# Performance work log

Measured on AMD Instinct MI355X. Metric: run time of the kernel, lower is better.

The kernel has to match this reference:

```python
import jax, jax.numpy as jnp
import numpy as np

N = 500000
D = 128
R = D // 4  # reduction = 4
G = 2048    # number of graphs


def setup_inputs() -> dict:
    key = jax.random.key(0)
    ks = jax.random.split(key, 8)
    x = jax.random.normal(ks[0], (N, D), dtype=jnp.float32)
    batch = jnp.sort(jax.random.randint(ks[1], (N,), 0, G))
    # SE-gate MLP params (nn.Linear stores weight as [out,in]; we store transposed for x @ W)
    fc_w1 = jax.random.normal(ks[2], (D, R), dtype=jnp.float32) * (1.0 / np.sqrt(D))
    fc_b1 = jnp.zeros((R,), dtype=jnp.float32)
    fc_w2 = jax.random.normal(ks[3], (R, D), dtype=jnp.float32) * (1.0 / np.sqrt(R))
    fc_b2 = jnp.zeros((D,), dtype=jnp.float32)
    # xavier-uniform weight_matrix [D, D]
    lim = np.sqrt(6.0 / (D + D))
    W = jax.random.uniform(ks[4], (D, D), dtype=jnp.float32, minval=-lim, maxval=lim)
    return {"x": x, "batch": batch, "size": G,
            "fc_w1": fc_w1, "fc_b1": fc_b1, "fc_w2": fc_w2, "fc_b2": fc_b2, "W": W}


def reference(x, batch, size, fc_w1, fc_b1, fc_w2, fc_b2, W):
    # gated SE-block: attention = tanh(MLP(x)); x = attention*x + x
    attention = jnp.tanh(jnp.maximum(x @ fc_w1 + fc_b1, 0.0) @ fc_w2 + fc_b2)
    x2 = attention * x + x  # [N, D]
    # global_mean_pool: segment mean over graphs
    seg_sum = jax.ops.segment_sum(x2, batch, num_segments=size)           # [G, D]
    counts = jax.ops.segment_sum(jnp.ones((x2.shape[0],), x2.dtype), batch, num_segments=size)
    mean = seg_sum / jnp.maximum(counts, 1.0)[:, None]                     # [G, D]
    transformed_global = jnp.tanh(mean @ W)                                # [G, D]
    # gather-broadcast per-graph global back to nodes, per-node attention coef
    coefs = jax.nn.sigmoid(jnp.sum(x2 * transformed_global[batch], axis=1))  # [N]
    weighted = coefs[:, None] * x2                                          # [N, D]
    return jax.ops.segment_sum(weighted, batch, num_segments=size)          # [G, D]
```

## Files before the change

kernel.cpp:

```cpp
#include <hip/hip_runtime.h>
#include <hip/hip_bf16.h>

#define DDIM 128
#define RDIM 32
#define PBLK 256
#define BLK  256
#define HSTR 40

typedef __attribute__((ext_vector_type(8))) short bf16x8;
typedef __attribute__((ext_vector_type(4))) float f32x4;

__device__ __forceinline__ float tanh_fast(float v) {
  float e = __expf(2.f * v);
  return 1.f - 2.f * __builtin_amdgcn_rcpf(e + 1.f);
}
__device__ __forceinline__ float sigmoid_fast(float v) {
  return __builtin_amdgcn_rcpf(1.f + __expf(-v));
}
__device__ __forceinline__ unsigned short f2bf(float f) {
  unsigned u = __float_as_uint(f);
  u += 0x7fffu + ((u >> 16) & 1u);
  return (unsigned short)(u >> 16);
}
__device__ __forceinline__ float bf2f(unsigned short s) {
  return __uint_as_float(((unsigned)s) << 16);
}
__device__ __forceinline__ unsigned pkbf(float lo, float hi) {
  __hip_bfloat162 t2 = __float22bfloat162_rn(make_float2(lo, hi));
  return *reinterpret_cast<unsigned*>(&t2);
}
__device__ __forceinline__ int lower_bound(const int* __restrict__ b, int n, int v) {
  int lo = 0, hi = n;
  while (lo < hi) { int m = (lo + hi) >> 1; if (b[m] < v) lo = m + 1; else hi = m; }
  return lo;
}

__global__ void k0_prep(const float* __restrict__ w1, const float* __restrict__ w2,
                        unsigned short* __restrict__ w1tf, unsigned short* __restrict__ w2tf)
{
  const int i  = blockIdx.x * blockDim.x + threadIdx.x;
  const int l  = i & 63;
  const int lr = l & 15, q = l >> 4;
  if (i < 512) {
    const int frag = i >> 6;
    const int mt2 = frag >> 2, kk = frag & 3;
    bf16x8 v;
    #pragma unroll
    for (int j = 0; j < 8; ++j)
      v[j] = (short)f2bf(w1[(size_t)(kk * 32 + q * 8 + j) * RDIM + mt2 * 16 + lr]);
    *(bf16x8*)&w1tf[(size_t)i * 8] = v;
  } else {
    const int mt = (i - 512) >> 6;
    bf16x8 v;
    #pragma unroll
    for (int j = 0; j < 8; ++j)
      v[j] = (short)f2bf(w2[(size_t)(q * 8 + j) * DDIM + mt * 16 + lr]);
    *(bf16x8*)&w2tf[(size_t)(i - 512) * 8] = v;
  }
}

__global__ void kb_bounds(const int* __restrict__ batch, int* __restrict__ bounds,
                          int N, int G)
{
  const int g = blockIdx.x * blockDim.x + threadIdx.x;
  if (g <= G) bounds[g] = lower_bound(batch, N, g);
}

__global__ __launch_bounds__(BLK, 2) void k_fused(
    const float* __restrict__ x,
    const unsigned short* __restrict__ w1tf, const float* __restrict__ b1,
    const unsigned short* __restrict__ w2tf, const float* __restrict__ b2,
    const float* __restrict__ W, const int* __restrict__ bounds,
    float* __restrict__ out, int N)
{
  __shared__ float ring[4][2][2048];
  __shared__ unsigned short hs4[4][16 * HSTR];
  __shared__ float part[4][132];
  __shared__ float meanv[DDIM];
  __shared__ float tgs[DDIM];

  const int t  = threadIdx.x;
  const int l  = t & 63;
  const int w  = t >> 6;
  const int lr = l & 15;
  const int q  = l >> 4;
  const int g  = blockIdx.x;
  const int lo = bounds[g], hi = bounds[g + 1];
  const int cnt = hi - lo;
  unsigned short* hs = hs4[w];

  if (cnt <= 0) { if (t < DDIM) out[(size_t)g * DDIM + t] = 0.f; return; }

  bf16x8 w1r[2][4], w2r[8];
  #pragma unroll
  for (int mt2 = 0; mt2 < 2; ++mt2)
    #pragma unroll
    for (int kk = 0; kk < 4; ++kk)
      w1r[mt2][kk] = *(const bf16x8*)&w1tf[(size_t)((mt2 * 4 + kk) * 64 + l) * 8];
  #pragma unroll
  for (int mt = 0; mt < 8; ++mt)
    w2r[mt] = *(const bf16x8*)&w2tf[(size_t)(mt * 64 + l) * 8];

  const int sr  = l >> 5;
  const int sc  = l & 31;
  const int swz = lr & 7;
  const int ntile = (cnt + 15) >> 4;

  auto fill = [&](int s, int tb) {
    float* lds = ring[w][s];
    #pragma unroll
    for (int j = 0; j < 8; ++j) {
      const int r   = j * 2 + sr;
      const int row = lo + min(tb + r, cnt - 1);
      const int lc  = sc ^ (r & 7);
      __builtin_amdgcn_global_load_lds(x + (size_t)row * DDIM + lc * 4,
                                       lds + j * 256, 16, 0, 0);
    }
  };

  auto mlp = [&](int s, float (&y)[8][4]) {
    float* lds = ring[w][s];
    bf16x8 xf[4];
    #pragma unroll
    for (int kk = 0; kk < 4; ++kk) {
      const int c0 = kk * 8 + q * 2;
      float4 a = *(const float4*)&lds[lr * 128 + ((c0    ) ^ swz) * 4];
      float4 b = *(const float4*)&lds[lr * 128 + ((c0 + 1) ^ swz) * 4];
      uint4 u;
      u.x = pkbf(a.x, a.y); u.y = pkbf(a.z, a.w);
      u.z = pkbf(b.x, b.y); u.w = pkbf(b.z, b.w);
      xf[kk] = *(bf16x8*)&u;
    }
    f32x4 hacc[2];
    {
      float4 bv0 = *(const float4*)(b1 + q * 4);
      float4 bv1 = *(const float4*)(b1 + 16 + q * 4);
      hacc[0][0] = bv0.x; hacc[0][1] = bv0.y; hacc[0][2] = bv0.z; hacc[0][3] = bv0.w;
      hacc[1][0] = bv1.x; hacc[1][1] = bv1.y; hacc[1][2] = bv1.z; hacc[1][3] = bv1.w;
    }
    #pragma unroll
    for (int kk = 0; kk < 4; ++kk) {
      hacc[0] = __builtin_amdgcn_mfma_f32_16x16x32_bf16(w1r[0][kk], xf[kk], hacc[0], 0, 0, 0);
      hacc[1] = __builtin_amdgcn_mfma_f32_16x16x32_bf16(w1r[1][kk], xf[kk], hacc[1], 0, 0, 0);
    }
    #pragma unroll
    for (int mt2 = 0; mt2 < 2; ++mt2) {
      float h0 = fmaxf(hacc[mt2][0], 0.f), h1 = fmaxf(hacc[mt2][1], 0.f);
      float h2 = fmaxf(hacc[mt2][2], 0.f), h3 = fmaxf(hacc[mt2][3], 0.f);
      uint2 p; p.x = pkbf(h0, h1); p.y = pkbf(h2, h3);
      *(uint2*)&hs[lr * HSTR + mt2 * 16 + q * 4] = p;
    }
    bf16x8 ah = *(const bf16x8*)&hs[lr * HSTR + q * 8];
    f32x4 cacc[8];
    #pragma unroll
    for (int mt = 0; mt < 8; ++mt) {
      float4 bv = *(const float4*)(b2 + mt * 16 + q * 4);
      cacc[mt][0] = bv.x; cacc[mt][1] = bv.y; cacc[mt][2] = bv.z; cacc[mt][3] = bv.w;
    }
    #pragma unroll
    for (int mt = 0; mt < 8; ++mt)
      cacc[mt] = __builtin_amdgcn_mfma_f32_16x16x32_bf16(w2r[mt], ah, cacc[mt], 0, 0, 0);
    #pragma unroll
    for (int mt = 0; mt < 8; ++mt) {
      float4 xg = *(const float4*)&lds[lr * 128 + ((mt * 4 + q) ^ swz) * 4];
      y[mt][0] = xg.x * (1.f + tanh_fast(cacc[mt][0]));
      y[mt][1] = xg.y * (1.f + tanh_fast(cacc[mt][1]));
      y[mt][2] = xg.z * (1.f + tanh_fast(cacc[mt][2]));
      y[mt][3] = xg.w * (1.f + tanh_fast(cacc[mt][3]));
    }
  };

  float macc[8][4];
  #pragma unroll
  for (int mt = 0; mt < 8; ++mt)
    #pragma unroll
    for (int c = 0; c < 4; ++c) macc[mt][c] = 0.f;

  {
    int ti = w, cur = 0;
    if (ti < ntile) fill(cur, ti * 16);
    for (; ti < ntile; ti += 4) {
      const int tn = ti + 4;
      if (tn < ntile) {
        fill(cur ^ 1, tn * 16);
        asm volatile("s_waitcnt vmcnt(8)" ::: "memory");
      } else {
        asm volatile("s_waitcnt vmcnt(0)" ::: "memory");
      }
      float y[8][4];
      mlp(cur, y);
      if (ti * 16 + lr < cnt) {
        #pragma unroll
        for (int mt = 0; mt < 8; ++mt)
          #pragma unroll
          for (int c = 0; c < 4; ++c) macc[mt][c] += y[mt][c];
      }
      cur ^= 1;
    }
  }
  __syncthreads();

  #pragma unroll
  for (int mt = 0; mt < 8; ++mt)
    #pragma unroll
    for (int c = 0; c < 4; ++c) {
      float v = macc[mt][c];
      v += __shfl_xor(v, 1, 64);
      v += __shfl_xor(v, 2, 64);
      v += __shfl_xor(v, 4, 64);
      v += __shfl_xor(v, 8, 64);
      macc[mt][c] = v;
    }
  if (lr == 0) {
    #pragma unroll
    for (int mt = 0; mt < 8; ++mt)
      *(float4*)&part[w][mt * 16 + q * 4] =
          make_float4(macc[mt][0], macc[mt][1], macc[mt][2], macc[mt][3]);
  }
  __syncthreads();
  if (t < DDIM) {
    float m = part[0][t] + part[1][t] + part[2][t] + part[3][t];
    meanv[t] = m / (float)cnt;
  }
  __syncthreads();

  {
    const int c = t & 127, s = t >> 7;
    float a = 0.f;
    #pragma unroll 8
    for (int k = 0; k < 64; ++k)
      a = fmaf(meanv[s * 64 + k], W[(size_t)(s * 64 + k) * DDIM + c], a);
    part[s][c] = a;
  }
  __syncthreads();
  if (t < DDIM) tgs[t] = tanh_fast(part[0][t] + part[1][t]);
  __syncthreads();

  float oacc[8][4];
  #pragma unroll
  for (int mt = 0; mt < 8; ++mt)
    #pragma unroll
    for (int c = 0; c < 4; ++c) oacc[mt][c] = 0.f;

  {
    int ti = w, cur = 0;
    if (ti < ntile) fill(cur, ti * 16);
    for (; ti < ntile; ti += 4) {
      const int tn = ti + 4;
      if (tn < ntile) {
        fill(cur ^ 1, tn * 16);
        asm volatile("s_waitcnt vmcnt(8)" ::: "memory");
      } else {
        asm volatile("s_waitcnt vmcnt(0)" ::: "memory");
      }
      float y[8][4];
      mlp(cur, y);
      float p = 0.f;
      #pragma unroll
      for (int mt = 0; mt < 8; ++mt) {
        float4 tg4 = *(const float4*)&tgs[mt * 16 + q * 4];
        p = fmaf(y[mt][0], tg4.x, p); p = fmaf(y[mt][1], tg4.y, p);
        p = fmaf(y[mt][2], tg4.z, p); p = fmaf(y[mt][3], tg4.w, p);
      }
      p += __shfl_xor(p, 16, 64);
      p += __shfl_xor(p, 32, 64);
      const float coef = sigmoid_fast(p);
      if (ti * 16 + lr < cnt) {
        #pragma unroll
        for (int mt = 0; mt < 8; ++mt)
          #pragma unroll
          for (int c = 0; c < 4; ++c)
            oacc[mt][c] = fmaf(coef, y[mt][c], oacc[mt][c]);
      }
      cur ^= 1;
    }
  }
  __syncthreads();

  #pragma unroll
  for (int mt = 0; mt < 8; ++mt)
    #pragma unroll
    for (int c = 0; c < 4; ++c) {
      float v = oacc[mt][c];
      v += __shfl_xor(v, 1, 64);
      v += __shfl_xor(v, 2, 64);
      v += __shfl_xor(v, 4, 64);
      v += __shfl_xor(v, 8, 64);
      oacc[mt][c] = v;
    }
  if (lr == 0) {
    #pragma unroll
    for (int mt = 0; mt < 8; ++mt)
      *(float4*)&part[w][mt * 16 + q * 4] =
          make_float4(oacc[mt][0], oacc[mt][1], oacc[mt][2], oacc[mt][3]);
  }
  __syncthreads();
  if (t < DDIM)
    out[(size_t)g * DDIM + t] = part[0][t] + part[1][t] + part[2][t] + part[3][t];
}

extern "C" void kernel_launch(void* const* d_in, const int* in_sizes, int n_in,
                              void* d_out, int out_size, void* d_ws, size_t ws_size,
                              hipStream_t stream) {
  const float* x     = (const float*)d_in[0];
  const int*   batch = (const int*)d_in[1];
  const float* w1 = (const float*)d_in[3];
  const float* b1 = (const float*)d_in[4];
  const float* w2 = (const float*)d_in[5];
  const float* b2 = (const float*)d_in[6];
  const float* W  = (const float*)d_in[7];
  float* out = (float*)d_out;

  const int N = in_sizes[0] / DDIM;
  const int G = out_size / DDIM;

  unsigned short* w1tf = (unsigned short*)d_ws;
  unsigned short* w2tf = w1tf + 4096;
  int* bounds = (int*)(w2tf + 4096);
  (void)ws_size; (void)n_in;

  hipLaunchKernelGGL(k0_prep, dim3(4), dim3(PBLK), 0, stream, w1, w2, w1tf, w2tf);
  hipLaunchKernelGGL(kb_bounds, dim3((G + 1 + PBLK - 1) / PBLK), dim3(PBLK), 0, stream,
                     batch, bounds, N, G);
  hipLaunchKernelGGL(k_fused, dim3(G), dim3(BLK), 0, stream,
                     x, w1tf, b1, w2tf, b2, W, bounds, out, N);
}
```

Measured before the change: 134.3 us.

## Move MLP weights to LDS and single-buffer tiles to raise occupancy

The per-wave double-buffered x ring becomes a single slot per wave. The next tile's async load is issued once the current tile has been copied into registers. The MLP weight fragments and b2 now live in shared memory instead of registers, and part/meanv alias the slot buffer. Launch bounds go from 2 to 3 blocks per CU and HSTR shrinks to 32, aiming for more resident waves to hide memory latency. The gating multiply now uses bf16-rounded x, which adds precision loss, and the extra LDS reads plus the HSTR change may add bank conflicts.

```diff
diff --git a/kernel.cpp b/kernel.cpp
--- a/kernel.cpp
+++ b/kernel.cpp
@@ -5,7 +5,7 @@
 #define RDIM 32
 #define PBLK 256
 #define BLK  256
-#define HSTR 40
+#define HSTR 32
 
 typedef __attribute__((ext_vector_type(8))) short bf16x8;
 typedef __attribute__((ext_vector_type(4))) float f32x4;
@@ -66,17 +66,18 @@
   if (g <= G) bounds[g] = lower_bound(batch, N, g);
 }
 
-__global__ __launch_bounds__(BLK, 2) void k_fused(
+__global__ __launch_bounds__(BLK, 3) void k_fused(
     const float* __restrict__ x,
     const unsigned short* __restrict__ w1tf, const float* __restrict__ b1,
     const unsigned short* __restrict__ w2tf, const float* __restrict__ b2,
     const float* __restrict__ W, const int* __restrict__ bounds,
     float* __restrict__ out, int N)
 {
-  __shared__ float ring[4][2][2048];
+  __shared__ unsigned short w1t[512 * 8];
+  __shared__ unsigned short w2t[512 * 8];
+  __shared__ float slots[4][2048];
   __shared__ unsigned short hs4[4][16 * HSTR];
-  __shared__ float part[4][132];
-  __shared__ float meanv[DDIM];
+  __shared__ float b2s[DDIM];
   __shared__ float tgs[DDIM];
 
   const int t  = threadIdx.x;
@@ -88,60 +89,66 @@
   const int lo = bounds[g], hi = bounds[g + 1];
   const int cnt = hi - lo;
   unsigned short* hs = hs4[w];
+  float* slot = slots[w];
+  float (*part)[132] = (float (*)[132])slots[0];
+  float* meanv = slots[1];
 
   if (cnt <= 0) { if (t < DDIM) out[(size_t)g * DDIM + t] = 0.f; return; }
 
-  bf16x8 w1r[2][4], w2r[8];
-  #pragma unroll
-  for (int mt2 = 0; mt2 < 2; ++mt2)
-    #pragma unroll
-    for (int kk = 0; kk < 4; ++kk)
-      w1r[mt2][kk] = *(const bf16x8*)&w1tf[(size_t)((mt2 * 4 + kk) * 64 + l) * 8];
-  #pragma unroll
-  for (int mt = 0; mt < 8; ++mt)
-    w2r[mt] = *(const bf16x8*)&w2tf[(size_t)(mt * 64 + l) * 8];
+  for (int i = t; i < 512; i += BLK) {
+    ((bf16x8*)w1t)[i] = ((const bf16x8*)w1tf)[i];
+    ((bf16x8*)w2t)[i] = ((const bf16x8*)w2tf)[i];
+  }
+  if (t < DDIM) b2s[t] = b2[t];
+  const float4 b1q0 = *(const float4*)(b1 + q * 4);
+  const float4 b1q1 = *(const float4*)(b1 + 16 + q * 4);
+  __syncthreads();
 
   const int sr  = l >> 5;
   const int sc  = l & 31;
   const int swz = lr & 7;
   const int ntile = (cnt + 15) >> 4;
 
-  auto fill = [&](int s, int tb) {
-    float* lds = ring[w][s];
+  auto fill = [&](int tb) {
     #pragma unroll
     for (int j = 0; j < 8; ++j) {
       const int r   = j * 2 + sr;
       const int row = lo + min(tb + r, cnt - 1);
       const int lc  = sc ^ (r & 7);
       __builtin_amdgcn_global_load_lds(x + (size_t)row * DDIM + lc * 4,
-                                       lds + j * 256, 16, 0, 0);
+                                       slot + j * 256, 16, 0, 0);
     }
   };
 
-  auto mlp = [&](int s, float (&y)[8][4]) {
-    float* lds = ring[w][s];
-    bf16x8 xf[4];
+  auto loadregs = [&](bf16x8 (&xf)[4], uint2 (&xg)[8]) {
     #pragma unroll
     for (int kk = 0; kk < 4; ++kk) {
       const int c0 = kk * 8 + q * 2;
-      float4 a = *(const float4*)&lds[lr * 128 + ((c0    ) ^ swz) * 4];
-      float4 b = *(const float4*)&lds[lr * 128 + ((c0 + 1) ^ swz) * 4];
+      float4 a = *(const float4*)&slot[lr * 128 + ((c0    ) ^ swz) * 4];
+      float4 b = *(const float4*)&slot[lr * 128 + ((c0 + 1) ^ swz) * 4];
       uint4 u;
       u.x = pkbf(a.x, a.y); u.y = pkbf(a.z, a.w);
       u.z = pkbf(b.x, b.y); u.w = pkbf(b.z, b.w);
       xf[kk] = *(bf16x8*)&u;
     }
+    #pragma unroll
+    for (int mt = 0; mt < 8; ++mt) {
+      float4 v = *(const float4*)&slot[lr * 128 + ((mt * 4 + q) ^ swz) * 4];
+      xg[mt].x = pkbf(v.x, v.y); xg[mt].y = pkbf(v.z, v.w);
+    }
+  };
+
+  auto compute = [&](const bf16x8 (&xf)[4], const uint2 (&xg)[8],
+                     f32x4 (&cacc)[8]) {
     f32x4 hacc[2];
-    {
-      float4 bv0 = *(const float4*)(b1 + q * 4);
-      float4 bv1 = *(const float4*)(b1 + 16 + q * 4);
-      hacc[0][0] = bv0.x; hacc[0][1] = bv0.y; hacc[0][2] = bv0.z; hacc[0][3] = bv0.w;
-      hacc[1][0] = bv1.x; hacc[1][1] = bv1.y; hacc[1][2] = bv1.z; hacc[1][3] = bv1.w;
-    }
+    hacc[0][0] = b1q0.x; hacc[0][1] = b1q0.y; hacc[0][2] = b1q0.z; hacc[0][3] = b1q0.w;
+    hacc[1][0] = b1q1.x; hacc[1][1] = b1q1.y; hacc[1][2] = b1q1.z; hacc[1][3] = b1q1.w;
     #pragma unroll
     for (int kk = 0; kk < 4; ++kk) {
-      hacc[0] = __builtin_amdgcn_mfma_f32_16x16x32_bf16(w1r[0][kk], xf[kk], hacc[0], 0, 0, 0);
-      hacc[1] = __builtin_amdgcn_mfma_f32_16x16x32_bf16(w1r[1][kk], xf[kk], hacc[1], 0, 0, 0);
+      bf16x8 wa = *(const bf16x8*)&w1t[(size_t)((0 * 4 + kk) * 64 + l) * 8];
+      bf16x8 wb = *(const bf16x8*)&w1t[(size_t)((1 * 4 + kk) * 64 + l) * 8];
+      hacc[0] = __builtin_amdgcn_mfma_f32_16x16x32_bf16(wa, xf[kk], hacc[0], 0, 0, 0);
+      hacc[1] = __builtin_amdgcn_mfma_f32_16x16x32_bf16(wb, xf[kk], hacc[1], 0, 0, 0);
     }
     #pragma unroll
     for (int mt2 = 0; mt2 < 2; ++mt2) {
@@ -151,22 +158,26 @@
       *(uint2*)&hs[lr * HSTR + mt2 * 16 + q * 4] = p;
     }
     bf16x8 ah = *(const bf16x8*)&hs[lr * HSTR + q * 8];
-    f32x4 cacc[8];
     #pragma unroll
     for (int mt = 0; mt < 8; ++mt) {
-      float4 bv = *(const float4*)(b2 + mt * 16 + q * 4);
+      float4 bv = *(const float4*)&b2s[mt * 16 + q * 4];
       cacc[mt][0] = bv.x; cacc[mt][1] = bv.y; cacc[mt][2] = bv.z; cacc[mt][3] = bv.w;
     }
     #pragma unroll
-    for (int mt = 0; mt < 8; ++mt)
-      cacc[mt] = __builtin_amdgcn_mfma_f32_16x16x32_bf16(w2r[mt], ah, cacc[mt], 0, 0, 0);
-    #pragma unroll
     for (int mt = 0; mt < 8; ++mt) {
-      float4 xg = *(const float4*)&lds[lr * 128 + ((mt * 4 + q) ^ swz) * 4];
-      y[mt][0] = xg.x * (1.f + tanh_fast(cacc[mt][0]));
-      y[mt][1] = xg.y * (1.f + tanh_fast(cacc[mt][1]));
-      y[mt][2] = xg.z * (1.f + tanh_fast(cacc[mt][2]));
-      y[mt][3] = xg.w * (1.f + tanh_fast(cacc[mt][3]));
+      bf16x8 wf = *(const bf16x8*)&w2t[(size_t)(mt * 64 + l) * 8];
+      cacc[mt] = __builtin_amdgcn_mfma_f32_16x16x32_bf16(wf, ah, cacc[mt], 0, 0, 0);
+    }
+    #pragma unroll
+    for (int mt = 0; mt < 8; ++mt) {
+      float x0 = bf2f((unsigned short)(xg[mt].x & 0xffffu));
+      float x1 = bf2f((unsigned short)(xg[mt].x >> 16));
+      float x2 = bf2f((unsigned short)(xg[mt].y & 0xffffu));
+      float x3 = bf2f((unsigned short)(xg[mt].y >> 16));
+      cacc[mt][0] = x0 * (1.f + tanh_fast(cacc[mt][0]));
+      cacc[mt][1] = x1 * (1.f + tanh_fast(cacc[mt][1]));
+      cacc[mt][2] = x2 * (1.f + tanh_fast(cacc[mt][2]));
+      cacc[mt][3] = x3 * (1.f + tanh_fast(cacc[mt][3]));
     }
   };
 
@@ -177,25 +188,22 @@
     for (int c = 0; c < 4; ++c) macc[mt][c] = 0.f;
 
   {
-    int ti = w, cur = 0;
-    if (ti < ntile) fill(cur, ti * 16);
+    int ti = w;
+    if (ti < ntile) fill(ti * 16);
     for (; ti < ntile; ti += 4) {
-      const int tn = ti + 4;
-      if (tn < ntile) {
-        fill(cur ^ 1, tn * 16);
-        asm volatile("s_waitcnt vmcnt(8)" ::: "memory");
-      } else {
-        asm volatile("s_waitcnt vmcnt(0)" ::: "memory");
-      }
-      float y[8][4];
-      mlp(cur, y);
+      asm volatile("s_waitcnt vmcnt(0)" ::: "memory");
+      bf16x8 xf[4]; uint2 xg[8];
+      loadregs(xf, xg);
+      asm volatile("s_waitcnt lgkmcnt(0)" ::: "memory");
+      if (ti + 4 < ntile) fill((ti + 4) * 16);
+      f32x4 cacc[8];
+      compute(xf, xg, cacc);
       if (ti * 16 + lr < cnt) {
         #pragma unroll
         for (int mt = 0; mt < 8; ++mt)
           #pragma unroll
-          for (int c = 0; c < 4; ++c) macc[mt][c] += y[mt][c];
+          for (int c = 0; c < 4; ++c) macc[mt][c] += cacc[mt][c];
       }
-      cur ^= 1;
     }
   }
   __syncthreads();
@@ -243,24 +251,22 @@
     for (int c = 0; c < 4; ++c) oacc[mt][c] = 0.f;
 
   {
-    int ti = w, cur = 0;
-    if (ti < ntile) fill(cur, ti * 16);
+    int ti = w;
+    if (ti < ntile) fill(ti * 16);
     for (; ti < ntile; ti += 4) {
-      const int tn = ti + 4;
-      if (tn < ntile) {
-        fill(cur ^ 1, tn * 16);
-        asm volatile("s_waitcnt vmcnt(8)" ::: "memory");
-      } else {
-        asm volatile("s_waitcnt vmcnt(0)" ::: "memory");
-      }
-      float y[8][4];
-      mlp(cur, y);
+      asm volatile("s_waitcnt vmcnt(0)" ::: "memory");
+      bf16x8 xf[4]; uint2 xg[8];
+      loadregs(xf, xg);
+      asm volatile("s_waitcnt lgkmcnt(0)" ::: "memory");
+      if (ti + 4 < ntile) fill((ti + 4) * 16);
+      f32x4 cacc[8];
+      compute(xf, xg, cacc);
       float p = 0.f;
       #pragma unroll
       for (int mt = 0; mt < 8; ++mt) {
         float4 tg4 = *(const float4*)&tgs[mt * 16 + q * 4];
-        p = fmaf(y[mt][0], tg4.x, p); p = fmaf(y[mt][1], tg4.y, p);
-        p = fmaf(y[mt][2], tg4.z, p); p = fmaf(y[mt][3], tg4.w, p);
+        p = fmaf(cacc[mt][0], tg4.x, p); p = fmaf(cacc[mt][1], tg4.y, p);
+        p = fmaf(cacc[mt][2], tg4.z, p); p = fmaf(cacc[mt][3], tg4.w, p);
       }
       p += __shfl_xor(p, 16, 64);
       p += __shfl_xor(p, 32, 64);
@@ -270,9 +276,8 @@
         for (int mt = 0; mt < 8; ++mt)
           #pragma unroll
           for (int c = 0; c < 4; ++c)
-            oacc[mt][c] = fmaf(coef, y[mt][c], oacc[mt][c]);
+            oacc[mt][c] = fmaf(coef, cacc[mt][c], oacc[mt][c]);
       }
-      cur ^= 1;
     }
   }
   __syncthreads();
```

New measurement: 150.9 us. +12.4%, slower.
